# Optimization experiments

Hardware: AMD Instinct MI355X
Metric: run time of the kernel (lower is better)

The kernel has to match this reference:

```python
import jax, jax.numpy as jnp
import numpy as np

N_EMBD = 1024
N_HEAD = 16

def setup_inputs() -> dict:
    key = jax.random.key(0)
    ks = jax.random.split(key, 5)
    x = jax.random.normal(ks[0], (4, 2048, N_EMBD), dtype=jnp.float32)
    # torch Linear default init ~ U(-1/sqrt(fan_in), 1/sqrt(fan_in)); use scaled normals
    s = 1.0 / np.sqrt(N_EMBD)
    W_attn = jax.random.normal(ks[1], (N_EMBD, 3 * N_EMBD), dtype=jnp.float32) * s
    b_attn = jax.random.normal(ks[2], (3 * N_EMBD,), dtype=jnp.float32) * s
    W_proj = jax.random.normal(ks[3], (N_EMBD, N_EMBD), dtype=jnp.float32) * s
    b_proj = jax.random.normal(ks[4], (N_EMBD,), dtype=jnp.float32) * s
    return {"x": x, "W_attn": W_attn, "b_attn": b_attn, "W_proj": W_proj, "b_proj": b_proj}

def reference(x, W_attn, b_attn, W_proj, b_proj) -> jnp.ndarray:
    B, T, C = x.shape
    H = N_HEAD
    D = C // H  # head dim
    qkv = x @ W_attn + b_attn  # [B,T,3C]
    q, k, v = jnp.split(qkv, 3, axis=-1)
    # [B,T,C] -> [B,H,T,D]
    q = q.reshape(B, T, H, D).transpose(0, 2, 1, 3)
    k = k.reshape(B, T, H, D).transpose(0, 2, 1, 3)
    v = v.reshape(B, T, H, D).transpose(0, 2, 1, 3)
    scale = 1.0 / jnp.sqrt(jnp.float32(D))
    att = jnp.einsum('bhqd,bhkd->bhqk', q, k) * scale  # [B,H,T,T]
    causal = jnp.tril(jnp.ones((T, T), dtype=bool))
    att = jnp.where(causal[None, None, :, :], att, -jnp.inf)
    att = jax.nn.softmax(att, axis=-1)
    y = jnp.einsum('bhqk,bhkd->bhqd', att, v)  # [B,H,T,D]
    y = y.transpose(0, 2, 1, 3).reshape(B, T, C)
    return y @ W_proj + b_proj
```

## Files before the change

kernel.cpp:

```cpp
#include <hip/hip_runtime.h>
#include <stdint.h>


typedef __attribute__((ext_vector_type(8))) short short8;
typedef __attribute__((ext_vector_type(4))) float floatx4;

#define AS1C(p) ((const __attribute__((address_space(1))) void*)(p))
#define AS3(p)  ((__attribute__((address_space(3))) void*)(p))

__device__ __forceinline__ unsigned short f2bf(float f) {
  unsigned int u = __builtin_bit_cast(unsigned int, f);
  u = (u + 0x7fffu + ((u >> 16) & 1u)) >> 16;
  return (unsigned short)u;
}
__device__ __forceinline__ unsigned short f2bf_trunc(float f) {
  return (unsigned short)(__builtin_bit_cast(unsigned int, f) >> 16);
}

__global__ void k_cvt(const float* __restrict__ in, unsigned short* __restrict__ out, int n4) {
  int i = blockIdx.x * blockDim.x + threadIdx.x;
  if (i < n4) {
    float4 v = ((const float4*)in)[i];
    ushort4 o;
    o.x = f2bf(v.x); o.y = f2bf(v.y); o.z = f2bf(v.z); o.w = f2bf(v.w);
    ((ushort4*)out)[i] = o;
  }
}

__global__ void k_tw(const float* __restrict__ in, unsigned short* __restrict__ out, int K, int N) {
  __shared__ float t[32][33];
  int n0 = blockIdx.x * 32, k0 = blockIdx.y * 32;
  int tx = threadIdx.x, ty = threadIdx.y;
#pragma unroll
  for (int i = 0; i < 4; i++)
    t[ty + 8 * i][tx] = in[(size_t)(k0 + ty + 8 * i) * N + n0 + tx];
  __syncthreads();
#pragma unroll
  for (int i = 0; i < 4; i++)
    out[(size_t)(n0 + ty + 8 * i) * K + k0 + tx] = f2bf(t[tx][ty + 8 * i]);
}

__global__ void k_tv(const unsigned short* __restrict__ qkv, unsigned short* __restrict__ vt) {
  __shared__ unsigned short t[32][33];
  int t0 = blockIdx.x * 32;
  int d0 = blockIdx.y * 32;
  int bh = blockIdx.z;
  int b = bh >> 4, h = bh & 15;
  int tx = threadIdx.x, ty = threadIdx.y;
#pragma unroll
  for (int i = 0; i < 4; i++)
    t[ty + 8 * i][tx] = qkv[(size_t)(b * 2048 + t0 + ty + 8 * i) * 3072 + 2048 + h * 64 + d0 + tx];
  __syncthreads();
#pragma unroll
  for (int i = 0; i < 4; i++)
    vt[(size_t)(bh * 64 + d0 + ty + 8 * i) * 2048 + t0 + tx] = t[tx][ty + 8 * i];
}

template <int OUT_F32>
__global__ __launch_bounds__(256)
void k_gemm(const unsigned short* __restrict__ A,
            const unsigned short* __restrict__ Bt,
            const float* __restrict__ bias,
            void* __restrict__ Cout, int M, int N, int K) {
  __shared__ unsigned short lA[128 * 64];
  __shared__ unsigned short lB[128 * 64];
  int tid = threadIdx.x;
  int lane = tid & 63, wv = tid >> 6;
  int lc = lane & 15, quad = lane >> 4;
  int m0 = blockIdx.y * 128, n0 = blockIdx.x * 128;
  int wm = (wv >> 1) * 64, wn = (wv & 1) * 64;
  int sw = lc & 7;

  floatx4 acc[4][4];
#pragma unroll
  for (int i = 0; i < 4; i++)
#pragma unroll
    for (int j = 0; j < 4; j++) acc[i][j] = (floatx4){0.f, 0.f, 0.f, 0.f};

  int srow = tid >> 3;
  int scol = (((tid & 7) ^ (srow & 7))) * 8;
  const unsigned short* gA = A + (size_t)(m0 + srow) * K + scol;
  const unsigned short* gB = Bt + (size_t)(n0 + srow) * K + scol;

  for (int k0 = 0; k0 < K; k0 += 64) {
#pragma unroll
    for (int c = 0; c < 4; c++) {
      __builtin_amdgcn_global_load_lds(AS1C(gA + (size_t)(32 * c) * K + k0),
                                       AS3(lA + (32 * c + 8 * wv) * 64), 16, 0, 0);
      __builtin_amdgcn_global_load_lds(AS1C(gB + (size_t)(32 * c) * K + k0),
                                       AS3(lB + (32 * c + 8 * wv) * 64), 16, 0, 0);
    }
    __syncthreads();
#pragma unroll
    for (int s = 0; s < 2; s++) {
      short8 af[4], bfr[4];
#pragma unroll
      for (int i = 0; i < 4; i++)
        af[i] = *(const short8*)(lA + (wm + i * 16 + lc) * 64 + (((s * 4 + quad) ^ sw) * 8));
#pragma unroll
      for (int j = 0; j < 4; j++)
        bfr[j] = *(const short8*)(lB + (wn + j * 16 + lc) * 64 + (((s * 4 + quad) ^ sw) * 8));
#pragma unroll
      for (int i = 0; i < 4; i++)
#pragma unroll
        for (int j = 0; j < 4; j++)
          acc[i][j] = __builtin_amdgcn_mfma_f32_16x16x32_bf16(af[i], bfr[j], acc[i][j], 0, 0, 0);
    }
    __syncthreads();
  }

  float bv[4];
#pragma unroll
  for (int j = 0; j < 4; j++) bv[j] = bias[n0 + wn + j * 16 + lc];
#pragma unroll
  for (int i = 0; i < 4; i++) {
#pragma unroll
    for (int j = 0; j < 4; j++) {
#pragma unroll
      for (int r = 0; r < 4; r++) {
        size_t idx = (size_t)(m0 + wm + i * 16 + quad * 4 + r) * N + (n0 + wn + j * 16 + lc);
        float v = acc[i][j][r] + bv[j];
        if (OUT_F32) ((float*)Cout)[idx] = v;
        else         ((unsigned short*)Cout)[idx] = f2bf(v);
      }
    }
  }
}

#define LP_STRIDE 68
__global__ __launch_bounds__(256, 4)
void k_flash(const unsigned short* __restrict__ qkv,
             const unsigned short* __restrict__ vt,
             unsigned short* __restrict__ y) {
  __shared__ unsigned short lK[64 * 64];
  __shared__ unsigned short lVT[64 * 64];
  __shared__ unsigned short lP[4][2][16 * LP_STRIDE];
  int tid = threadIdx.x, lane = tid & 63, wv = tid >> 6;
  int lc = lane & 15, quad = lane >> 4;
  int sw = lc & 7;
  int j  = blockIdx.x;
  int bh = blockIdx.y;
  int b = bh >> 4, h = bh & 15;
  int qtA = j, qtB = 31 - j;
  int qrA = qtA * 64 + wv * 16;
  int qrB = qtB * 64 + wv * 16;

  short8 qfA[2], qfB[2];
  {
    const unsigned short* qp = qkv + (size_t)(b * 2048 + qrA + lc) * 3072 + h * 64 + quad * 8;
    qfA[0] = *(const short8*)qp;
    qfA[1] = *(const short8*)(qp + 32);
  }
  {
    const unsigned short* qp = qkv + (size_t)(b * 2048 + qrB + lc) * 3072 + h * 64 + quad * 8;
    qfB[0] = *(const short8*)qp;
    qfB[1] = *(const short8*)(qp + 32);
  }

  float rsA[4] = {0.f, 0.f, 0.f, 0.f}, rsB[4] = {0.f, 0.f, 0.f, 0.f};
  floatx4 oA[4], oB[4];
#pragma unroll
  for (int dt = 0; dt < 4; dt++) {
    oA[dt] = (floatx4){0.f, 0.f, 0.f, 0.f};
    oB[dt] = (floatx4){0.f, 0.f, 0.f, 0.f};
  }

  int srow = tid >> 3;
  int scol = ((tid & 7) ^ (srow & 7)) * 8;
  const unsigned short* gK = qkv + (size_t)(b * 2048 + srow) * 3072 + 1024 + h * 64 + scol;
  const unsigned short* gV = vt + (size_t)(bh * 64 + srow) * 2048 + scol;

  const float SC2 = 0.18033688011f;
  int nt = qtB + 1;

  for (int kv = 0; kv < nt; kv++) {
    int kv0 = kv * 64;
#pragma unroll
    for (int c = 0; c < 2; c++) {
      __builtin_amdgcn_global_load_lds(AS1C(gK + (size_t)(kv0 + 32 * c) * 3072),
                                       AS3(lK + (32 * c + 8 * wv) * 64), 16, 0, 0);
      __builtin_amdgcn_global_load_lds(AS1C(gV + (size_t)(32 * c) * 2048 + kv0),
                                       AS3(lVT + (32 * c + 8 * wv) * 64), 16, 0, 0);
    }
    __syncthreads();

    bool withA = (kv <= qtA);

    floatx4 sB[4], sA[4];
#pragma unroll
    for (int n = 0; n < 4; n++) {
      short8 kf0 = *(const short8*)(lK + (n * 16 + lc) * 64 + ((quad ^ sw) * 8));
      short8 kf1 = *(const short8*)(lK + (n * 16 + lc) * 64 + (((4 + quad) ^ sw) * 8));
      floatx4 t = (floatx4){0.f, 0.f, 0.f, 0.f};
      t = __builtin_amdgcn_mfma_f32_16x16x32_bf16(qfB[0], kf0, t, 0, 0, 0);
      t = __builtin_amdgcn_mfma_f32_16x16x32_bf16(qfB[1], kf1, t, 0, 0, 0);
      sB[n] = t;
      if (withA) {
        floatx4 u = (floatx4){0.f, 0.f, 0.f, 0.f};
        u = __builtin_amdgcn_mfma_f32_16x16x32_bf16(qfA[0], kf0, u, 0, 0, 0);
        u = __builtin_amdgcn_mfma_f32_16x16x32_bf16(qfA[1], kf1, u, 0, 0, 0);
        sA[n] = u;
      }
    }

    {
      bool diag = (kv == qtB);
#pragma unroll
      for (int n = 0; n < 4; n++)
#pragma unroll
        for (int r = 0; r < 4; r++) {
          float arg = sB[n][r] * SC2;
          if (diag && (kv0 + n * 16 + lc > qrB + quad * 4 + r)) arg = -__builtin_inff();
          float p = __builtin_amdgcn_exp2f(arg);
          rsB[r] += p;
          lP[wv][0][(quad * 4 + r) * LP_STRIDE + n * 16 + lc] = f2bf_trunc(p);
        }
    }
    if (withA) {
      bool diag = (kv == qtA);
#pragma unroll
      for (int n = 0; n < 4; n++)
#pragma unroll
        for (int r = 0; r < 4; r++) {
          float arg = sA[n][r] * SC2;
          if (diag && (kv0 + n * 16 + lc > qrA + quad * 4 + r)) arg = -__builtin_inff();
          float p = __builtin_amdgcn_exp2f(arg);
          rsA[r] += p;
          lP[wv][1][(quad * 4 + r) * LP_STRIDE + n * 16 + lc] = f2bf_trunc(p);
        }
    }

#pragma unroll
    for (int s2 = 0; s2 < 2; s2++) {
      short8 pfB = *(const short8*)(&lP[wv][0][0] + lc * LP_STRIDE + s2 * 32 + quad * 8);
      short8 pfA;
      if (withA) pfA = *(const short8*)(&lP[wv][1][0] + lc * LP_STRIDE + s2 * 32 + quad * 8);
#pragma unroll
      for (int dt = 0; dt < 4; dt++) {
        short8 vf = *(const short8*)(lVT + (dt * 16 + lc) * 64 + (((s2 * 4 + quad) ^ sw) * 8));
        oB[dt] = __builtin_amdgcn_mfma_f32_16x16x32_bf16(pfB, vf, oB[dt], 0, 0, 0);
        if (withA) oA[dt] = __builtin_amdgcn_mfma_f32_16x16x32_bf16(pfA, vf, oA[dt], 0, 0, 0);
      }
    }
    __syncthreads();
  }

#pragma unroll
  for (int off = 1; off < 16; off <<= 1)
#pragma unroll
    for (int r = 0; r < 4; r++) {
      rsA[r] += __shfl_xor(rsA[r], off);
      rsB[r] += __shfl_xor(rsB[r], off);
    }
#pragma unroll
  for (int r = 0; r < 4; r++) {
    float invA = 1.0f / rsA[r];
    float invB = 1.0f / rsB[r];
#pragma unroll
    for (int dt = 0; dt < 4; dt++) {
      size_t ia = (size_t)(b * 2048 + qrA + quad * 4 + r) * 1024 + h * 64 + dt * 16 + lc;
      size_t ib = (size_t)(b * 2048 + qrB + quad * 4 + r) * 1024 + h * 64 + dt * 16 + lc;
      y[ia] = f2bf(oA[dt][r] * invA);
      y[ib] = f2bf(oB[dt][r] * invB);
    }
  }
}

extern "C" void kernel_launch(void* const* d_in, const int* in_sizes, int n_in,
                              void* d_out, int out_size, void* d_ws, size_t ws_size,
                              hipStream_t stream) {
  const float* x      = (const float*)d_in[0];
  const float* W_attn = (const float*)d_in[1];
  const float* b_attn = (const float*)d_in[2];
  const float* W_proj = (const float*)d_in[3];
  const float* b_proj = (const float*)d_in[4];

  char* ws = (char*)d_ws;
  unsigned short* xb     = (unsigned short*)ws;
  unsigned short* wattnT = (unsigned short*)(ws + 16777216);
  unsigned short* wprojT = (unsigned short*)(ws + 23068672);
  unsigned short* qkv    = (unsigned short*)(ws + 25165824);
  unsigned short* vt     = (unsigned short*)(ws + 75497472);
  unsigned short* y      = xb;

  k_cvt<<<8192, 256, 0, stream>>>(x, xb, 8388608 / 4);
  k_tw<<<dim3(96, 32), dim3(32, 8), 0, stream>>>(W_attn, wattnT, 1024, 3072);
  k_tw<<<dim3(32, 32), dim3(32, 8), 0, stream>>>(W_proj, wprojT, 1024, 1024);
  k_gemm<0><<<dim3(24, 64), 256, 0, stream>>>(xb, wattnT, b_attn, qkv, 8192, 3072, 1024);
  k_tv<<<dim3(64, 2, 64), dim3(32, 8), 0, stream>>>(qkv, vt);
  k_flash<<<dim3(16, 64), 256, 0, stream>>>(qkv, vt, y);
  k_gemm<1><<<dim3(8, 64), 256, 0, stream>>>(y, wprojT, b_proj, d_out, 8192, 1024, 1024);
}
```

Measured before the change: 271.3 us.

## Rewrite GEMM as 256x128 double-buffered 8-wave kernel with XCD-aware tile remap

```diff
diff --git a/kernel.cpp b/kernel.cpp
--- a/kernel.cpp
+++ b/kernel.cpp
@@ -7,6 +7,7 @@
 
 #define AS1C(p) ((const __attribute__((address_space(1))) void*)(p))
 #define AS3(p)  ((__attribute__((address_space(3))) void*)(p))
+#define GL16(src, dst) __builtin_amdgcn_global_load_lds(AS1C(src), AS3(dst), 16, 0, 0)
 
 __device__ __forceinline__ unsigned short f2bf(float f) {
   unsigned int u = __builtin_bit_cast(unsigned int, f);
@@ -57,20 +58,29 @@
 }
 
 template <int OUT_F32>
-__global__ __launch_bounds__(256)
-void k_gemm(const unsigned short* __restrict__ A,
-            const unsigned short* __restrict__ Bt,
-            const float* __restrict__ bias,
-            void* __restrict__ Cout, int M, int N, int K) {
-  __shared__ unsigned short lA[128 * 64];
-  __shared__ unsigned short lB[128 * 64];
+__global__ __launch_bounds__(512, 2)
+void k_gemm8(const unsigned short* __restrict__ A,
+             const unsigned short* __restrict__ Bt,
+             const float* __restrict__ bias,
+             void* __restrict__ Cout, int M, int N, int K) {
+  __shared__ unsigned short lA[2][256 * 64];
+  __shared__ unsigned short lB[2][128 * 64];
   int tid = threadIdx.x;
   int lane = tid & 63, wv = tid >> 6;
   int lc = lane & 15, quad = lane >> 4;
-  int m0 = blockIdx.y * 128, n0 = blockIdx.x * 128;
-  int wm = (wv >> 1) * 64, wn = (wv & 1) * 64;
   int sw = lc & 7;
 
+  unsigned nbx = gridDim.x;
+  unsigned nwg = nbx * gridDim.y;
+  unsigned flat = blockIdx.y * nbx + blockIdx.x;
+  unsigned cpx = nwg >> 3;
+  unsigned tile = (flat & 7u) * cpx + (flat >> 3);
+  int n0 = (int)(tile % nbx) * 128;
+  int m0 = (int)(tile / nbx) * 256;
+
+  int wm = (wv >> 1) * 64;
+  int wn = (wv & 1) * 64;
+
   floatx4 acc[4][4];
 #pragma unroll
   for (int i = 0; i < 4; i++)
@@ -78,35 +88,83 @@
     for (int j = 0; j < 4; j++) acc[i][j] = (floatx4){0.f, 0.f, 0.f, 0.f};
 
   int srow = tid >> 3;
-  int scol = (((tid & 7) ^ (srow & 7))) * 8;
+  int scol = ((tid & 7) ^ (srow & 7)) * 8;
   const unsigned short* gA = A + (size_t)(m0 + srow) * K + scol;
   const unsigned short* gB = Bt + (size_t)(n0 + srow) * K + scol;
 
-  for (int k0 = 0; k0 < K; k0 += 64) {
-#pragma unroll
-    for (int c = 0; c < 4; c++) {
-      __builtin_amdgcn_global_load_lds(AS1C(gA + (size_t)(32 * c) * K + k0),
-                                       AS3(lA + (32 * c + 8 * wv) * 64), 16, 0, 0);
-      __builtin_amdgcn_global_load_lds(AS1C(gB + (size_t)(32 * c) * K + k0),
-                                       AS3(lB + (32 * c + 8 * wv) * 64), 16, 0, 0);
-    }
-    __syncthreads();
-#pragma unroll
-    for (int s = 0; s < 2; s++) {
-      short8 af[4], bfr[4];
+  int NT = K >> 6;
+
+#pragma unroll
+  for (int i = 0; i < 4; i++)
+    GL16(gA + (size_t)(i * 64) * K, &lA[0][i * 4096 + wv * 512]);
+#pragma unroll
+  for (int i = 0; i < 2; i++)
+    GL16(gB + (size_t)(i * 64) * K, &lB[0][i * 4096 + wv * 512]);
+
+  for (int t = 0; t < NT; t++) {
+    const unsigned short* bufA = lA[t & 1];
+    const unsigned short* bufB = lB[t & 1];
+
+    if (t + 1 < NT) {
+      unsigned short* nA = lA[(t + 1) & 1];
+      unsigned short* nB = lB[(t + 1) & 1];
+      int k0 = (t + 1) << 6;
 #pragma unroll
       for (int i = 0; i < 4; i++)
-        af[i] = *(const short8*)(lA + (wm + i * 16 + lc) * 64 + (((s * 4 + quad) ^ sw) * 8));
-#pragma unroll
-      for (int j = 0; j < 4; j++)
-        bfr[j] = *(const short8*)(lB + (wn + j * 16 + lc) * 64 + (((s * 4 + quad) ^ sw) * 8));
-#pragma unroll
-      for (int i = 0; i < 4; i++)
-#pragma unroll
-        for (int j = 0; j < 4; j++)
-          acc[i][j] = __builtin_amdgcn_mfma_f32_16x16x32_bf16(af[i], bfr[j], acc[i][j], 0, 0, 0);
-    }
-    __syncthreads();
+        GL16(gA + (size_t)(i * 64) * K + k0, nA + i * 4096 + wv * 512);
+#pragma unroll
+      for (int i = 0; i < 2; i++)
+        GL16(gB + (size_t)(i * 64) * K + k0, nB + i * 4096 + wv * 512);
+      asm volatile("s_waitcnt vmcnt(6)" ::: "memory");
+    } else {
+      asm volatile("s_waitcnt vmcnt(0)" ::: "memory");
+    }
+    __builtin_amdgcn_s_barrier();
+    asm volatile("" ::: "memory");
+
+    short8 af[4][2];
+#pragma unroll
+    for (int m = 0; m < 4; m++)
+#pragma unroll
+      for (int ks = 0; ks < 2; ks++)
+        af[m][ks] = *(const short8*)(bufA + (wm + m * 16 + lc) * 64 + (((ks * 4 + quad) ^ sw) * 8));
+    short8 bf0[2][2];
+#pragma unroll
+    for (int n = 0; n < 2; n++)
+#pragma unroll
+      for (int ks = 0; ks < 2; ks++)
+        bf0[n][ks] = *(const short8*)(bufB + (wn + n * 16 + lc) * 64 + (((ks * 4 + quad) ^ sw) * 8));
+    __builtin_amdgcn_s_setprio(1);
+#pragma unroll
+    for (int m = 0; m < 4; m++)
+#pragma unroll
+      for (int n = 0; n < 2; n++)
+#pragma unroll
+        for (int ks = 0; ks < 2; ks++)
+          acc[m][n] = __builtin_amdgcn_mfma_f32_16x16x32_bf16(af[m][ks], bf0[n][ks], acc[m][n], 0, 0, 0);
+    __builtin_amdgcn_s_setprio(0);
+    asm volatile("" ::: "memory");
+    __builtin_amdgcn_s_barrier();
+    asm volatile("" ::: "memory");
+
+    short8 bf1[2][2];
+#pragma unroll
+    for (int n = 0; n < 2; n++)
+#pragma unroll
+      for (int ks = 0; ks < 2; ks++)
+        bf1[n][ks] = *(const short8*)(bufB + (wn + (n + 2) * 16 + lc) * 64 + (((ks * 4 + quad) ^ sw) * 8));
+    __builtin_amdgcn_s_setprio(1);
+#pragma unroll
+    for (int m = 0; m < 4; m++)
+#pragma unroll
+      for (int n = 0; n < 2; n++)
+#pragma unroll
+        for (int ks = 0; ks < 2; ks++)
+          acc[m][n + 2] = __builtin_amdgcn_mfma_f32_16x16x32_bf16(af[m][ks], bf1[n][ks], acc[m][n + 2], 0, 0, 0);
+    __builtin_amdgcn_s_setprio(0);
+    asm volatile("" ::: "memory");
+    __builtin_amdgcn_s_barrier();
+    asm volatile("" ::: "memory");
   }
 
   float bv[4];
@@ -286,8 +344,8 @@
   k_cvt<<<8192, 256, 0, stream>>>(x, xb, 8388608 / 4);
   k_tw<<<dim3(96, 32), dim3(32, 8), 0, stream>>>(W_attn, wattnT, 1024, 3072);
   k_tw<<<dim3(32, 32), dim3(32, 8), 0, stream>>>(W_proj, wprojT, 1024, 1024);
-  k_gemm<0><<<dim3(24, 64), 256, 0, stream>>>(xb, wattnT, b_attn, qkv, 8192, 3072, 1024);
+  k_gemm8<0><<<dim3(24, 32), 512, 0, stream>>>(xb, wattnT, b_attn, qkv, 8192, 3072, 1024);
   k_tv<<<dim3(64, 2, 64), dim3(32, 8), 0, stream>>>(qkv, vt);
   k_flash<<<dim3(16, 64), 256, 0, stream>>>(qkv, vt, y);
-  k_gemm<1><<<dim3(8, 64), 256, 0, stream>>>(y, wprojT, b_proj, d_out, 8192, 1024, 1024);
-}
+  k_gemm8<1><<<dim3(8, 32), 512, 0, stream>>>(y, wprojT, b_proj, d_out, 8192, 1024, 1024);
+}
```

Measured after the change: 280.9 us. 3.5% more time.
